# Performance work log

Measured on AMD Instinct MI355X. Metric: run time of the kernel, lower is better.

The kernel has to match this reference:

```python
import jax, jax.numpy as jnp
import numpy as np

# ---- batched 6-qubit state-vector simulator ----

def _apply_b(state, gate, wire):
    # per-sample gate: gate (B,2,2), state (B,)+(2,)*w
    B = state.shape[0]; w = state.ndim - 1
    pre = 2 ** wire; post = 2 ** (w - wire - 1)
    s = state.reshape(B, pre, 2, post)
    s = jnp.einsum('bij,bpjq->bpiq', gate, s)
    return s.reshape(state.shape)

def _apply_s(state, gate, wire):
    # shared gate: gate (2,2)
    B = state.shape[0]; w = state.ndim - 1
    pre = 2 ** wire; post = 2 ** (w - wire - 1)
    s = state.reshape(B, pre, 2, post)
    s = jnp.einsum('ij,bpjq->bpiq', gate, s)
    return s.reshape(state.shape)

def _cnot(state, ctrl, tgt):
    s0 = jnp.take(state, 0, axis=1 + ctrl)
    s1 = jnp.take(state, 1, axis=1 + ctrl)
    t_ax = 1 + tgt if tgt < ctrl else tgt  # target axis after removing ctrl axis
    s1 = jnp.flip(s1, axis=t_ax)
    return jnp.stack([s0, s1], axis=1 + ctrl)

def _ry(t):
    c = jnp.cos(t / 2); s = jnp.sin(t / 2)
    return jnp.stack([jnp.stack([c, -s], -1), jnp.stack([s, c], -1)], -2).astype(jnp.complex64)

def _rz(t):
    e = jnp.exp(-0.5j * t.astype(jnp.complex64))
    z = jnp.zeros_like(e)
    return jnp.stack([jnp.stack([e, z], -1), jnp.stack([z, jnp.conj(e)], -1)], -2)

def _rx(t):
    c = jnp.cos(t / 2).astype(jnp.complex64)
    s = (-1j * jnp.sin(t / 2)).astype(jnp.complex64)
    return jnp.stack([jnp.stack([c, s], -1), jnp.stack([s, c], -1)], -2)

def _expvals_z(state):
    p = state.real ** 2 + state.imag ** 2  # (B,)+(2,)*w probabilities
    w = state.ndim - 1
    outs = []
    for i in range(w):
        axes = tuple(a for a in range(1, w + 1) if a != i + 1)
        m = p.sum(axis=axes)  # (B,2) marginal on wire i
        outs.append(m[:, 0] - m[:, 1])
    return jnp.stack(outs, axis=1)  # (B, w) -- matches torch.stack(outputs).T

def _circuit(x, weights):
    # x: (B, w) rescaled features, weights: (layers, 3*w)
    B, w = x.shape
    layers = weights.shape[0]
    e1 = jnp.arctan(x)        # featue_function_1
    e2 = jnp.arctan(x * x)    # featue_function_2 ('atan' type)
    state = jnp.zeros((B,) + (2,) * w, jnp.complex64).at[(slice(None),) + (0,) * w].set(1.0)
    for i in range(w):
        state = _apply_b(state, _ry(e1[:, i]), i)  # AngleEmbedding rotation='Y'
    for i in range(w):
        state = _apply_b(state, _rz(e2[:, i]), i)  # AngleEmbedding rotation='Z'
    for l in range(layers):
        for i in range(w):
            state = _cnot(state, i, (i + 1) % w)
        for i in range(w):
            state = _cnot(state, i, (i + 2) % w)
        for i in range(w):
            state = _apply_s(state, _rx(weights[l, 3 * i + 0]), i)
            state = _apply_s(state, _ry(weights[l, 3 * i + 1]), i)
            state = _apply_s(state, _rz(weights[l, 3 * i + 2]), i)
    return _expvals_z(state)

def _forward(x, phi, Wc, bc):
    Bsz = x.shape[0]
    w = Wc.shape[0]
    sig = jax.nn.sigmoid

    def step(carry, x_t):
        c, h = carry
        z = jnp.concatenate([x_t, h], axis=1)          # torch.hstack([input[:,i], h])
        X = 2.0 * sig(z @ Wc.T + bc) - 1.0             # feature_combiner + rescale
        f_t = sig(_circuit(X, phi[0]))
        i_t = sig(_circuit(X, phi[1]))
        C_t = sig(_circuit(X, phi[2]))
        o_t = sig(_circuit(X, phi[3]))
        c_new = f_t * c + i_t * C_t
        rescaled = o_t * jnp.tanh(c_new)
        h_new = _circuit(rescaled, phi[4])
        y_t = _circuit(rescaled, phi[5])
        return (c_new, h_new), y_t

    init = (jnp.zeros((Bsz, w), jnp.float32), jnp.zeros((Bsz, w), jnp.float32))
    (c, h), ys = jax.lax.scan(jax.checkpoint(step), init, jnp.swapaxes(x, 0, 1))
    return jnp.swapaxes(ys, 0, 1), c, h  # y_out (B,T,w), (c, h)

def setup_inputs() -> dict:
    key = jax.random.key(0)
    k1, k2, k3, k4 = jax.random.split(key, 4)
    x = jax.random.normal(k1, (512, 256, 8), jnp.float32)
    phi = jax.random.normal(k2, (6, 2, 18), jnp.float32) / jnp.sqrt(jnp.float32(2.0))  # std 1/sqrt(layers)
    bound = float(1.0 / np.sqrt(8 + 6))  # Linear(feature_dim+wires, wires) default init
    Wc = jax.random.uniform(k3, (6, 14), jnp.float32, -bound, bound)
    bc = jax.random.uniform(k4, (6,), jnp.float32, -bound, bound)
    return {"x": x, "phi": phi, "Wc": Wc, "bc": bc}

def reference(x, phi, Wc, bc):
    return _forward(x, phi, Wc, bc)
```

## Files before the change

### kernel.cpp

```cpp
#include <hip/hip_runtime.h>


namespace {

constexpr int BATCH  = 512;
constexpr int TSTEPS = 256;

__device__ __forceinline__ float sigf(float v) { return 1.0f / (1.0f + __expf(-v)); }
__device__ __forceinline__ float tanh_fast(float v) { return 1.0f - 2.0f / (1.0f + __expf(v + v)); }

__device__ __forceinline__ float rl(float v, int l) {
  return __int_as_float(__builtin_amdgcn_readlane(__float_as_int(v), l));
}

template<int M>
__device__ __forceinline__ float shx(float v, int lane4) {
  if constexpr (M < 32) {
    return __int_as_float(__builtin_amdgcn_ds_swizzle(__float_as_int(v), 0x1F | (M << 10)));
  } else {
    return __int_as_float(__builtin_amdgcn_ds_bpermute(lane4 ^ (M << 2), __float_as_int(v)));
  }
}

template<int M1, int M2, int M12>
__device__ __forceinline__ void stage(float& ar, float& ai, float4 kA, float4 kB, int lane4) {
  float v1r = shx<M1>(ar, lane4),  v1i = shx<M1>(ai, lane4);
  float v2r = shx<M2>(ar, lane4),  v2i = shx<M2>(ai, lane4);
  float v3r = shx<M12>(ar, lane4), v3i = shx<M12>(ai, lane4);
  float nr = kA.x * ar;
  nr = fmaf(-kA.y, ai,  nr); nr = fmaf(kA.z, v1r, nr); nr = fmaf(-kA.w, v1i, nr);
  nr = fmaf( kB.x, v2r, nr); nr = fmaf(-kB.y, v2i, nr);
  nr = fmaf( kB.z, v3r, nr); nr = fmaf(-kB.w, v3i, nr);
  float ni = kA.x * ai;
  ni = fmaf(kA.y, ar,  ni); ni = fmaf(kA.z, v1i, ni); ni = fmaf(kA.w, v1r, ni);
  ni = fmaf(kB.x, v2i, ni); ni = fmaf(kB.y, v2r, ni);
  ni = fmaf(kB.z, v3i, ni); ni = fmaf(kB.w, v3r, ni);
  ar = nr; ai = ni;
}

__device__ __forceinline__ void gate_chain(float& ar, float& ai,
    const float4 (&kA)[6], const float4 (&kB)[6], int lane4) {
  stage<0x0F,0x1E,0x11>(ar, ai, kA[0], kB[0], lane4);
  stage<0x3C,0x3B,0x07>(ar, ai, kA[1], kB[1], lane4);
  stage<0x3F,0x3D,0x02>(ar, ai, kA[2], kB[2], lane4);
  stage<0x16,0x26,0x30>(ar, ai, kA[3], kB[3], lane4);
  stage<0x05,0x28,0x2D>(ar, ai, kA[4], kB[4], lane4);
  stage<0x14,0x0A,0x1E>(ar, ai, kA[5], kB[5], lane4);
}

__device__ __forceinline__ float expvals(float ar, float ai, const float (&fs)[9],
                                         int lane4, int gaddr) {
  float p  = fmaf(ar, ar, ai * ai);
  float pa = shx<1>(p, lane4), pb = shx<2>(p, lane4), pc = shx<3>(p, lane4);
  p = fmaf(fs[0], p, fmaf(fs[1], pa, fmaf(fs[2], pb, pc)));
  pa = shx<4>(p, lane4); pb = shx<8>(p, lane4); pc = shx<12>(p, lane4);
  p = fmaf(fs[3], p, fmaf(fs[4], pa, fmaf(fs[5], pb, pc)));
  pa = shx<16>(p, lane4); pb = shx<32>(p, lane4); pc = shx<48>(p, lane4);
  p = fmaf(fs[6], p, fmaf(fs[7], pa, fmaf(fs[8], pb, pc)));
  return __int_as_float(__builtin_amdgcn_ds_bpermute(gaddr, __float_as_int(p)));
}

__device__ __forceinline__ void trig(float Xv, float& A_, float& B_, float& C_, float& D_) {
  float tq   = Xv * Xv;
  float cth1 = rsqrtf(1.f + tq);
  float sth1 = Xv * cth1;
  float u1   = 1.f + cth1, r1 = rsqrtf(u1 + u1);
  float c1   = u1 * r1,    s1 = sth1 * r1;
  float tq2  = tq * tq;
  float cth2 = rsqrtf(1.f + tq2);
  float sth2 = tq * cth2;
  float u2   = 1.f + cth2, r2 = rsqrtf(u2 + u2);
  float c2   = u2 * r2,    s2 = sth2 * r2;
  A_ = c1 * c2; B_ = c1 * s2; C_ = s1 * c2; D_ = s1 * s2;
}

__device__ __forceinline__ void embed(float A_, float B_, float C_, float D_,
                                      int lane, float& ar, float& ai) {
  {
    float Aj = rl(A_,0), Bj = rl(B_,0), Cj = rl(C_,0), Dj = rl(D_,0);
    bool bj = lane & 1;
    ar = bj ? Cj : Aj;
    ai = bj ? Dj : -Bj;
  }
#pragma unroll
  for (int jj = 1; jj < 6; ++jj) {
    float Aj = rl(A_,jj), Bj = rl(B_,jj), Cj = rl(C_,jj), Dj = rl(D_,jj);
    bool bj = (lane >> jj) & 1;
    float fr = bj ? Cj : Aj;
    float fi = bj ? Dj : -Bj;
    float nr = ar * fr - ai * fi;
    ai = fmaf(ar, fi, ai * fr);
    ar = nr;
  }
}

__device__ __forceinline__ void make_K(const float4* fgc, int lane,
                                       float4 (&kA)[6], float4 (&kB)[6]) {
  constexpr unsigned BM[2][6] = {
    {0x18,0x30,0x39,0x0C,0x26,0x33},
    {0x2A,0x15,0x01,0x35,0x3A,0x3D}};
#pragma unroll
  for (int s = 0; s < 6; ++s) {
    int l = s / 3, i0 = (s % 3) * 2;
    float4 ga1 = fgc[(l*6+i0)*2],     gb1 = fgc[(l*6+i0)*2+1];
    float4 ga2 = fgc[(l*6+i0+1)*2],   gb2 = fgc[(l*6+i0+1)*2+1];
    bool p1 = __popc(lane & (int)BM[l][i0])   & 1;
    bool p2 = __popc(lane & (int)BM[l][i0+1]) & 1;
    float arr = p1 ? gb1.z : ga1.x, ari = p1 ? gb1.w : ga1.y;
    float brr = p1 ? gb1.x : ga1.z, bri = p1 ? gb1.y : ga1.w;
    float crr = p2 ? gb2.z : ga2.x, cri = p2 ? gb2.w : ga2.y;
    float drr = p2 ? gb2.x : ga2.z, dri = p2 ? gb2.y : ga2.w;
    kA[s] = make_float4(crr*arr - cri*ari, crr*ari + cri*arr,
                        crr*brr - cri*bri, crr*bri + cri*brr);
    kB[s] = make_float4(drr*arr - dri*ari, drr*ari + dri*arr,
                        drr*brr - dri*bri, drr*bri + dri*brr);
  }
}

#define PACK_IDX ((0x2AULL)|(0x15ULL<<6)|(0x01ULL<<12)|(0x35ULL<<18)|(0x3AULL<<24)|(0x3DULL<<30))

}

__global__ __launch_bounds__(256, 2)
void qlstm_kernel(const float* __restrict__ x, const float* __restrict__ phi,
                  const float* __restrict__ Wc, const float* __restrict__ bc,
                  float* __restrict__ out)
{
  __shared__ float4 fG[144];
  __shared__ float4 gates4[6];
  __shared__ float  h_s[6];

  const int tid   = threadIdx.x;
  const int wave  = tid >> 6;
  const int lane  = tid & 63;
  const int lane4 = lane << 2;
  const int b     = blockIdx.x;

  if (tid < 72) {
    int g = tid / 12, rem = tid % 12, l = rem / 6, i = rem % 6;
    const float* w = phi + g*36 + l*18 + i*3;
    float sa, ca, sb, cb, sc, cc;
    sincosf(0.5f * w[0], &sa, &ca);
    sincosf(0.5f * w[1], &sb, &cb);
    sincosf(0.5f * w[2], &sc, &cc);
    float m00r =  cb*ca, m00i =  sb*sa;
    float m01r = -sb*ca, m01i = -cb*sa;
    float m10r =  sb*ca, m10i = -cb*sa;
    float m11r =  cb*ca, m11i = -sb*sa;
    float4 A, Bv;
    A.x  = m00r*cc + m00i*sc;  A.y  = m00i*cc - m00r*sc;
    A.z  = m01r*cc + m01i*sc;  A.w  = m01i*cc - m01r*sc;
    Bv.x = m10r*cc - m10i*sc;  Bv.y = m10i*cc + m10r*sc;
    Bv.z = m11r*cc - m11i*sc;  Bv.w = m11i*cc + m11r*sc;
    fG[2*tid] = A; fG[2*tid+1] = Bv;
  }
  if (tid < 6) h_s[tid] = 0.f;
  __syncthreads();

  const int j = (lane < 6) ? lane : 0;
  float Wr[14];
#pragma unroll
  for (int k = 0; k < 14; ++k) Wr[k] = Wc[j*14 + k];
  const float bcj = bc[j];

  float sg0 = (lane & 1)  ? -1.f : 1.f;
  float sg1 = (lane & 2)  ? -1.f : 1.f;
  float sg2 = (lane & 4)  ? -1.f : 1.f;
  float sg3 = (lane & 8)  ? -1.f : 1.f;
  float sg4 = (lane & 16) ? -1.f : 1.f;
  float sg5 = (lane & 32) ? -1.f : 1.f;
  float fs[9] = { sg0*sg1, sg1, sg0,  sg2*sg3, sg3, sg2,  sg4*sg5, sg5, sg4 };

  int sh    = (lane < 6) ? (6 * lane) : 0;
  int gaddr = (int)((PACK_IDX >> sh) & 63ULL) << 2;

  float4 kA1[6], kB1[6], kA2[6], kB2[6];
  make_K(&fG[wave * 24], lane, kA1, kB1);
  make_K(&fG[(4 + (wave & 1)) * 24], lane, kA2, kB2);

  float c_sc  = 0.f;
  float hlast = 0.f;

  const float* xbase = x + (size_t)b * TSTEPS * 8;
  float4 xa = *(const float4*)(xbase);
  float4 xb = *(const float4*)(xbase + 4);

  for (int t = 0; t < TSTEPS; ++t) {
    float hv0 = h_s[0], hv1 = h_s[1], hv2 = h_s[2];
    float hv3 = h_s[3], hv4 = h_s[4], hv5 = h_s[5];
    float acc = bcj;
    acc = fmaf(xa.x, Wr[0],  acc); acc = fmaf(xa.y, Wr[1],  acc);
    acc = fmaf(xa.z, Wr[2],  acc); acc = fmaf(xa.w, Wr[3],  acc);
    acc = fmaf(xb.x, Wr[4],  acc); acc = fmaf(xb.y, Wr[5],  acc);
    acc = fmaf(xb.z, Wr[6],  acc); acc = fmaf(xb.w, Wr[7],  acc);
    acc = fmaf(hv0,  Wr[8],  acc); acc = fmaf(hv1,  Wr[9],  acc);
    acc = fmaf(hv2,  Wr[10], acc); acc = fmaf(hv3,  Wr[11], acc);
    acc = fmaf(hv4,  Wr[12], acc); acc = fmaf(hv5,  Wr[13], acc);
    float Xj = 1.f - 2.f / (1.f + __expf(acc));

    int tn = (t + 1 < TSTEPS) ? (t + 1) : t;
    float4 xa_n = *(const float4*)(xbase + (size_t)tn * 8);
    float4 xb_n = *(const float4*)(xbase + (size_t)tn * 8 + 4);

    float A_, B_, C_, D_;
    trig(Xj, A_, B_, C_, D_);
    float ar, ai;
    embed(A_, B_, C_, D_, lane, ar, ai);
    gate_chain(ar, ai, kA1, kB1, lane4);
    float Wv  = expvals(ar, ai, fs, lane4, gaddr);
    float sgv = sigf(Wv);
    if (lane < 6) ((float*)&gates4[lane])[wave] = sgv;
    __syncthreads();

    if (wave < 2) {
      float4 g4 = gates4[j];
      float cn  = fmaf(g4.x, c_sc, g4.y * g4.z);
      c_sc = cn;
      float resc = g4.w * tanh_fast(cn);
      float A2, B2, C2, D2;
      trig(resc, A2, B2, C2, D2);
      float ar2, ai2;
      embed(A2, B2, C2, D2, lane, ar2, ai2);
      gate_chain(ar2, ai2, kA2, kB2, lane4);
      float Wv2 = expvals(ar2, ai2, fs, lane4, gaddr);
      if (wave == 0) {
        if (lane < 6) h_s[lane] = Wv2;
        hlast = Wv2;
      } else if (lane < 6) {
        out[((size_t)b * TSTEPS + t) * 6 + lane] = Wv2;
      }
    }
    xa = xa_n; xb = xb_n;
    __syncthreads();
  }

  if (wave == 0 && lane < 6) {
    size_t cbase = (size_t)BATCH * TSTEPS * 6;
    out[cbase + (size_t)b * 6 + lane] = c_sc;
    out[cbase + (size_t)BATCH * 6 + (size_t)b * 6 + lane] = hlast;
  }
}

extern "C" void kernel_launch(void* const* d_in, const int* in_sizes, int n_in,
                              void* d_out, int out_size, void* d_ws, size_t ws_size,
                              hipStream_t stream) {
  const float* x   = (const float*)d_in[0];
  const float* phi = (const float*)d_in[1];
  const float* Wc  = (const float*)d_in[2];
  const float* bc  = (const float*)d_in[3];
  float* out = (float*)d_out;
  (void)in_sizes; (void)n_in; (void)out_size; (void)d_ws; (void)ws_size;
  hipLaunchKernelGGL(qlstm_kernel, dim3(BATCH), dim3(256), 0, stream,
                     x, phi, Wc, bc, out);
}
```

Before: 559.8 us.

## Packed float2 complex math, LDS-based embedding broadcast, and pinned gate registers

Rewrites the per-stage complex gate updates using two-wide float vectors so the compiler can emit packed FMA instructions. The embedding factors are now written to a small per-wave LDS buffer and read back instead of being broadcast with 24 readlane calls, and they are refactored into an (E+sgn*F) form that removes the selects. Gate coefficients and weights are pinned in VGPRs with empty asm, and the launch bounds move to explicit waves-per-EU attributes. The LDS round-trip relies on intra-wave ordering with no barrier, and the asm pinning adds register pressure.

```diff
diff --git a/kernel.cpp b/kernel.cpp
--- a/kernel.cpp
+++ b/kernel.cpp
@@ -6,12 +6,13 @@
 constexpr int BATCH  = 512;
 constexpr int TSTEPS = 256;
 
+typedef float v2f __attribute__((ext_vector_type(2)));
+
+__device__ __forceinline__ v2f splat2(float s) { v2f r; r.x = s; r.y = s; return r; }
+__device__ __forceinline__ v2f cswapneg(v2f v) { v2f r; r.x = -v.y; r.y = v.x; return r; }
+
 __device__ __forceinline__ float sigf(float v) { return 1.0f / (1.0f + __expf(-v)); }
 __device__ __forceinline__ float tanh_fast(float v) { return 1.0f - 2.0f / (1.0f + __expf(v + v)); }
-
-__device__ __forceinline__ float rl(float v, int l) {
-  return __int_as_float(__builtin_amdgcn_readlane(__float_as_int(v), l));
-}
 
 template<int M>
 __device__ __forceinline__ float shx(float v, int lane4) {
@@ -23,34 +24,35 @@
 }
 
 template<int M1, int M2, int M12>
-__device__ __forceinline__ void stage(float& ar, float& ai, float4 kA, float4 kB, int lane4) {
-  float v1r = shx<M1>(ar, lane4),  v1i = shx<M1>(ai, lane4);
-  float v2r = shx<M2>(ar, lane4),  v2i = shx<M2>(ai, lane4);
-  float v3r = shx<M12>(ar, lane4), v3i = shx<M12>(ai, lane4);
-  float nr = kA.x * ar;
-  nr = fmaf(-kA.y, ai,  nr); nr = fmaf(kA.z, v1r, nr); nr = fmaf(-kA.w, v1i, nr);
-  nr = fmaf( kB.x, v2r, nr); nr = fmaf(-kB.y, v2i, nr);
-  nr = fmaf( kB.z, v3r, nr); nr = fmaf(-kB.w, v3i, nr);
-  float ni = kA.x * ai;
-  ni = fmaf(kA.y, ar,  ni); ni = fmaf(kA.z, v1i, ni); ni = fmaf(kA.w, v1r, ni);
-  ni = fmaf(kB.x, v2i, ni); ni = fmaf(kB.y, v2r, ni);
-  ni = fmaf(kB.z, v3i, ni); ni = fmaf(kB.w, v3r, ni);
-  ar = nr; ai = ni;
-}
-
-__device__ __forceinline__ void gate_chain(float& ar, float& ai,
+__device__ __forceinline__ void stagep(v2f& s, float4 kA, float4 kB, int lane4) {
+  v2f v1, v2, v3;
+  v1.x = shx<M1>(s.x, lane4);  v1.y = shx<M1>(s.y, lane4);
+  v2.x = shx<M2>(s.x, lane4);  v2.y = shx<M2>(s.y, lane4);
+  v3.x = shx<M12>(s.x, lane4); v3.y = shx<M12>(s.y, lane4);
+  v2f u = splat2(kA.x) * s;
+  u = __builtin_elementwise_fma(splat2(kA.y), cswapneg(s),  u);
+  u = __builtin_elementwise_fma(splat2(kA.z), v1,           u);
+  u = __builtin_elementwise_fma(splat2(kA.w), cswapneg(v1), u);
+  u = __builtin_elementwise_fma(splat2(kB.x), v2,           u);
+  u = __builtin_elementwise_fma(splat2(kB.y), cswapneg(v2), u);
+  u = __builtin_elementwise_fma(splat2(kB.z), v3,           u);
+  u = __builtin_elementwise_fma(splat2(kB.w), cswapneg(v3), u);
+  s = u;
+}
+
+__device__ __forceinline__ void gate_chain(v2f& s,
     const float4 (&kA)[6], const float4 (&kB)[6], int lane4) {
-  stage<0x0F,0x1E,0x11>(ar, ai, kA[0], kB[0], lane4);
-  stage<0x3C,0x3B,0x07>(ar, ai, kA[1], kB[1], lane4);
-  stage<0x3F,0x3D,0x02>(ar, ai, kA[2], kB[2], lane4);
-  stage<0x16,0x26,0x30>(ar, ai, kA[3], kB[3], lane4);
-  stage<0x05,0x28,0x2D>(ar, ai, kA[4], kB[4], lane4);
-  stage<0x14,0x0A,0x1E>(ar, ai, kA[5], kB[5], lane4);
-}
-
-__device__ __forceinline__ float expvals(float ar, float ai, const float (&fs)[9],
+  stagep<0x0F,0x1E,0x11>(s, kA[0], kB[0], lane4);
+  stagep<0x3C,0x3B,0x07>(s, kA[1], kB[1], lane4);
+  stagep<0x3F,0x3D,0x02>(s, kA[2], kB[2], lane4);
+  stagep<0x16,0x26,0x30>(s, kA[3], kB[3], lane4);
+  stagep<0x05,0x28,0x2D>(s, kA[4], kB[4], lane4);
+  stagep<0x14,0x0A,0x1E>(s, kA[5], kB[5], lane4);
+}
+
+__device__ __forceinline__ float expvals(v2f s, const float (&fs)[9],
                                          int lane4, int gaddr) {
-  float p  = fmaf(ar, ar, ai * ai);
+  float p  = fmaf(s.x, s.x, s.y * s.y);
   float pa = shx<1>(p, lane4), pb = shx<2>(p, lane4), pc = shx<3>(p, lane4);
   p = fmaf(fs[0], p, fmaf(fs[1], pa, fmaf(fs[2], pb, pc)));
   pa = shx<4>(p, lane4); pb = shx<8>(p, lane4); pc = shx<12>(p, lane4);
@@ -60,7 +62,7 @@
   return __int_as_float(__builtin_amdgcn_ds_bpermute(gaddr, __float_as_int(p)));
 }
 
-__device__ __forceinline__ void trig(float Xv, float& A_, float& B_, float& C_, float& D_) {
+__device__ __forceinline__ float4 trigEF(float Xv) {
   float tq   = Xv * Xv;
   float cth1 = rsqrtf(1.f + tq);
   float sth1 = Xv * cth1;
@@ -71,27 +73,25 @@
   float sth2 = tq * cth2;
   float u2   = 1.f + cth2, r2 = rsqrtf(u2 + u2);
   float c2   = u2 * r2,    s2 = sth2 * r2;
-  A_ = c1 * c2; B_ = c1 * s2; C_ = s1 * c2; D_ = s1 * s2;
-}
-
-__device__ __forceinline__ void embed(float A_, float B_, float C_, float D_,
-                                      int lane, float& ar, float& ai) {
-  {
-    float Aj = rl(A_,0), Bj = rl(B_,0), Cj = rl(C_,0), Dj = rl(D_,0);
-    bool bj = lane & 1;
-    ar = bj ? Cj : Aj;
-    ai = bj ? Dj : -Bj;
-  }
-#pragma unroll
-  for (int jj = 1; jj < 6; ++jj) {
-    float Aj = rl(A_,jj), Bj = rl(B_,jj), Cj = rl(C_,jj), Dj = rl(D_,jj);
-    bool bj = (lane >> jj) & 1;
-    float fr = bj ? Cj : Aj;
-    float fi = bj ? Dj : -Bj;
-    float nr = ar * fr - ai * fi;
-    ai = fmaf(ar, fi, ai * fr);
-    ar = nr;
-  }
+  float up = 0.5f * (c1 + s1), um = 0.5f * (c1 - s1);
+  return make_float4(c2 * up, -s2 * um, c2 * um, -s2 * up);
+}
+
+__device__ __forceinline__ v2f embedEF(const float4* __restrict__ efw,
+                                       const float (&sgn)[6]) {
+  float4 e0 = efw[0];
+  v2f s;
+  s.x = fmaf(sgn[0], e0.z, e0.x);
+  s.y = fmaf(sgn[0], e0.w, e0.y);
+#pragma unroll
+  for (int k = 1; k < 6; ++k) {
+    float4 e = efw[k];
+    float fr = fmaf(sgn[k], e.z, e.x);
+    float fi = fmaf(sgn[k], e.w, e.y);
+    v2f t = splat2(fr) * s;
+    s = __builtin_elementwise_fma(splat2(fi), cswapneg(s), t);
+  }
+  return s;
 }
 
 __device__ __forceinline__ void make_K(const float4* fgc, int lane,
@@ -118,15 +118,18 @@
 }
 
 #define PACK_IDX ((0x2AULL)|(0x15ULL<<6)|(0x01ULL<<12)|(0x35ULL<<18)|(0x3AULL<<24)|(0x3DULL<<30))
-
-}
-
-__global__ __launch_bounds__(256, 2)
+#define PIN4(v) asm volatile("" : "+v"((v).x), "+v"((v).y), "+v"((v).z), "+v"((v).w))
+
+}
+
+__global__ __attribute__((amdgpu_flat_work_group_size(256, 256)))
+           __attribute__((amdgpu_waves_per_eu(2, 2)))
 void qlstm_kernel(const float* __restrict__ x, const float* __restrict__ phi,
                   const float* __restrict__ Wc, const float* __restrict__ bc,
                   float* __restrict__ out)
 {
   __shared__ float4 fG[144];
+  __shared__ float4 ef_s[4][8];
   __shared__ float4 gates4[6];
   __shared__ float  h_s[6];
 
@@ -163,13 +166,12 @@
   for (int k = 0; k < 14; ++k) Wr[k] = Wc[j*14 + k];
   const float bcj = bc[j];
 
-  float sg0 = (lane & 1)  ? -1.f : 1.f;
-  float sg1 = (lane & 2)  ? -1.f : 1.f;
-  float sg2 = (lane & 4)  ? -1.f : 1.f;
-  float sg3 = (lane & 8)  ? -1.f : 1.f;
-  float sg4 = (lane & 16) ? -1.f : 1.f;
-  float sg5 = (lane & 32) ? -1.f : 1.f;
-  float fs[9] = { sg0*sg1, sg1, sg0,  sg2*sg3, sg3, sg2,  sg4*sg5, sg5, sg4 };
+  float sgn[6];
+#pragma unroll
+  for (int k = 0; k < 6; ++k) sgn[k] = ((lane >> k) & 1) ? -1.f : 1.f;
+  float fs[9] = { sgn[0]*sgn[1], sgn[1], sgn[0],
+                  sgn[2]*sgn[3], sgn[3], sgn[2],
+                  sgn[4]*sgn[5], sgn[5], sgn[4] };
 
   int sh    = (lane < 6) ? (6 * lane) : 0;
   int gaddr = (int)((PACK_IDX >> sh) & 63ULL) << 2;
@@ -177,6 +179,10 @@
   float4 kA1[6], kB1[6], kA2[6], kB2[6];
   make_K(&fG[wave * 24], lane, kA1, kB1);
   make_K(&fG[(4 + (wave & 1)) * 24], lane, kA2, kB2);
+#pragma unroll
+  for (int s = 0; s < 6; ++s) { PIN4(kA1[s]); PIN4(kB1[s]); PIN4(kA2[s]); PIN4(kB2[s]); }
+#pragma unroll
+  for (int k = 0; k < 14; ++k) asm volatile("" : "+v"(Wr[k]));
 
   float c_sc  = 0.f;
   float hlast = 0.f;
@@ -184,6 +190,8 @@
   const float* xbase = x + (size_t)b * TSTEPS * 8;
   float4 xa = *(const float4*)(xbase);
   float4 xb = *(const float4*)(xbase + 4);
+
+  float4* efw = &ef_s[wave][0];
 
   for (int t = 0; t < TSTEPS; ++t) {
     float hv0 = h_s[0], hv1 = h_s[1], hv2 = h_s[2];
@@ -202,12 +210,11 @@
     float4 xa_n = *(const float4*)(xbase + (size_t)tn * 8);
     float4 xb_n = *(const float4*)(xbase + (size_t)tn * 8 + 4);
 
-    float A_, B_, C_, D_;
-    trig(Xj, A_, B_, C_, D_);
-    float ar, ai;
-    embed(A_, B_, C_, D_, lane, ar, ai);
-    gate_chain(ar, ai, kA1, kB1, lane4);
-    float Wv  = expvals(ar, ai, fs, lane4, gaddr);
+    float4 ef = trigEF(Xj);
+    if (lane < 6) efw[lane] = ef;
+    v2f s = embedEF(efw, sgn);
+    gate_chain(s, kA1, kB1, lane4);
+    float Wv  = expvals(s, fs, lane4, gaddr);
     float sgv = sigf(Wv);
     if (lane < 6) ((float*)&gates4[lane])[wave] = sgv;
     __syncthreads();
@@ -217,12 +224,11 @@
       float cn  = fmaf(g4.x, c_sc, g4.y * g4.z);
       c_sc = cn;
       float resc = g4.w * tanh_fast(cn);
-      float A2, B2, C2, D2;
-      trig(resc, A2, B2, C2, D2);
-      float ar2, ai2;
-      embed(A2, B2, C2, D2, lane, ar2, ai2);
-      gate_chain(ar2, ai2, kA2, kB2, lane4);
-      float Wv2 = expvals(ar2, ai2, fs, lane4, gaddr);
+      float4 ef2 = trigEF(resc);
+      if (lane < 6) efw[lane] = ef2;
+      v2f s2 = embedEF(efw, sgn);
+      gate_chain(s2, kA2, kB2, lane4);
+      float Wv2 = expvals(s2, fs, lane4, gaddr);
       if (wave == 0) {
         if (lane < 6) h_s[lane] = Wv2;
         hlast = Wv2;
```

Result: slower. 604.2 us (+7.9%).
